# Kernel optimization log

Measured on AMD Instinct MI355X. Metric: run time of the kernel, lower is better.

Reference implementation:

```python
import jax, jax.numpy as jnp
import numpy as np

LN_EPS = 1e-5
MIN_MASK_SUM = 1e-6


def setup_inputs() -> dict:
    key = jax.random.key(0)
    ks = jax.random.split(key, 8)
    B, N, D = 8, 576, 1024
    K, H, W = 64, 512, 512
    OUT, GEOM = 256, 5
    feature_map = jax.random.normal(ks[0], (B, N, D), dtype=jnp.float32)
    masks = jax.random.randint(ks[1], (B, K, H, W), 0, 2).astype(bool)
    s = 0.02
    w1 = jax.random.normal(ks[2], (D + GEOM, OUT), dtype=jnp.float32) * s
    b1 = jnp.zeros((OUT,), dtype=jnp.float32)
    ln_g = jnp.ones((OUT,), dtype=jnp.float32)
    ln_b = jnp.zeros((OUT,), dtype=jnp.float32)
    w2 = jax.random.normal(ks[3], (OUT, OUT), dtype=jnp.float32) * s
    b2 = jnp.zeros((OUT,), dtype=jnp.float32)
    return {"feature_map": feature_map, "masks": masks, "w1": w1, "b1": b1,
            "ln_g": ln_g, "ln_b": ln_b, "w2": w2, "b2": b2}


def _geom(masks):
    # masks: [B,K,H,W] bool -> [B,K,5] (cx, cy, area_norm, bbox_w, bbox_h)
    B, K, H, W = masks.shape
    mf = masks.astype(jnp.float32)
    area = mf.sum((-2, -1))                                  # [B,K]
    xg = jnp.arange(W, dtype=jnp.float32)
    yg = jnp.arange(H, dtype=jnp.float32)
    safe = jnp.maximum(area, 1.0)
    cx = jnp.einsum('bkhw,w->bk', mf, xg) / safe / W
    cy = jnp.einsum('bkhw,h->bk', mf, yg) / safe / H
    xs_any = masks.any(axis=2)                               # [B,K,W]
    ys_any = masks.any(axis=3)                               # [B,K,H]
    xi = jnp.arange(W, dtype=jnp.int32)
    yi = jnp.arange(H, dtype=jnp.int32)
    BIG = jnp.int32(1 << 30)
    xmin = jnp.min(jnp.where(xs_any, xi, BIG), -1)
    xmax = jnp.max(jnp.where(xs_any, xi, -1), -1)
    ymin = jnp.min(jnp.where(ys_any, yi, BIG), -1)
    ymax = jnp.max(jnp.where(ys_any, yi, -1), -1)
    bw = (xmax - xmin + 1).astype(jnp.float32) / W
    bh = (ymax - ymin + 1).astype(jnp.float32) / H
    geom = jnp.stack([cx, cy, area / (H * W), bw, bh], -1)   # [B,K,5]
    return jnp.where((area >= 1.0)[..., None], geom, 0.0)


def reference(feature_map, masks, w1, b1, ln_g, ln_b, w2, b2):
    B, N, D = feature_map.shape
    _, K, H, W = masks.shape
    Hf = int(round(N ** 0.5))
    # nearest-neighbor downsample of masks to the patch grid (torch 'nearest')
    ri = (jnp.arange(Hf) * H) // Hf
    ci = (jnp.arange(Hf) * W) // Hf
    m_small = masks[:, :, ri][:, :, :, ci].astype(jnp.float32).reshape(B, K, -1)  # [B,K,N]
    msum = jnp.maximum(m_small.sum(-1, keepdims=True), MIN_MASK_SUM)
    pooled = jnp.einsum('bkn,bnd->bkd', m_small, feature_map) / msum              # [B,K,D]
    pooled = pooled - feature_map.mean(axis=1, keepdims=True)                     # bg subtract
    geom = _geom(masks)                                                           # [B,K,5]
    x = jnp.concatenate([pooled, geom], axis=-1)                                  # [B,K,D+5]
    h = jax.nn.gelu(x @ w1 + b1, approximate=False)
    mu = h.mean(-1, keepdims=True)
    var = jnp.mean((h - mu) ** 2, axis=-1, keepdims=True)
    h = (h - mu) * jax.lax.rsqrt(var + LN_EPS) * ln_g + ln_b
    return h @ w2 + b2                                                            # [B,K,out]
```

## Files before the change

kernel.cpp:

```cpp
#include <hip/hip_runtime.h>
#include <math.h>

#define BB 8
#define NN 576
#define DD 1024
#define KK 64
#define HH 512
#define WW 512
#define OUTD 256
#define HF 24
#define XSTRIDE 1032

typedef int iv4 __attribute__((ext_vector_type(4)));

__global__ __launch_bounds__(1024) void k_geom(const int* __restrict__ masks,
                                               const float* __restrict__ fm,
                                               float* __restrict__ xbuf) {
    int bid = blockIdx.x;
    int b = bid & 7;
    int k = bid >> 3;
    int bk = b * KK + k;
    int tid = threadIdx.x;
    const int* mb = masks + (size_t)bk * (HH * WW);
    const iv4* mp = (const iv4*)mb;

    __shared__ float ms[NN];
    __shared__ float s_inv;
    __shared__ float rsum[16];

    float msv = 0.f;
    if (tid < NN) {
        int i = tid / HF, j = tid - i * HF;
        int ri = (i * HH) / HF, ci = (j * WW) / HF;
        msv = (mb[ri * WW + ci] != 0) ? 1.f : 0.f;
        ms[tid] = msv;
    }
    {
        float v = msv;
        for (int off = 32; off > 0; off >>= 1) v += __shfl_down(v, off);
        if ((tid & 63) == 0) rsum[tid >> 6] = v;
    }
    __syncthreads();
    if (tid == 0) {
        float s = 0.f;
        for (int i = 0; i < 16; ++i) s += rsum[i];
        s_inv = 1.0f / fmaxf(s, 1e-6f);
    }
    __syncthreads();

    const int y0 = tid >> 7;
    const int xb = (tid & 127) << 2;
    int cnt = 0, w3a = 0, syr = 0, colany = 0;
    int ymn_it = 1 << 20, ymx_it = -1;
    float acc = 0.f, facc = 0.f;

    auto STREAM = [&]() {
        #pragma unroll 8
        for (int it = 0; it < 64; ++it) {
            iv4 m = __builtin_nontemporal_load(&mp[tid + (it << 10)]);
            int sum4 = m.x + m.y + m.z + m.w;
            int mask4 = m.x | (m.y << 1) | (m.z << 2) | (m.w << 3);
            cnt += sum4;
            w3a += m.y + (m.z << 1) + ((m.w << 1) + m.w);
            syr += sum4 * it;
            colany |= mask4;
            if (mask4) { ymn_it = min(ymn_it, it); ymx_it = it; }
        }
    };
    auto POOL = [&]() {
        const float* fp = fm + (size_t)b * NN * DD + tid;
        for (int n = 0; n < NN; n += 4) {
            float4 mq = *(const float4*)&ms[n];
            float f0 = fp[(size_t)(n + 0) * DD];
            float f1 = fp[(size_t)(n + 1) * DD];
            float f2 = fp[(size_t)(n + 2) * DD];
            float f3 = fp[(size_t)(n + 3) * DD];
            facc += f0 + f1 + f2 + f3;
            acc = fmaf(mq.x, f0, acc);
            acc = fmaf(mq.y, f1, acc);
            acc = fmaf(mq.z, f2, acc);
            acc = fmaf(mq.w, f3, acc);
        }
    };

    if (((bid ^ (bid >> 8)) & 1) == 0) { STREAM(); POOL(); }
    else                               { POOL(); STREAM(); }

    {
        float* xp = xbuf + (size_t)bk * XSTRIDE;
        xp[tid] = acc * s_inv - facc * (1.0f / 576.0f);
    }

    int sx = xb * cnt + w3a;
    int sy = (syr << 3) + y0 * cnt;
    int xmn = colany ? xb + __builtin_ctz((unsigned)colany) : (1 << 30);
    int xmx = colany ? xb + (31 - __builtin_clz((unsigned)colany)) : -1;
    int ymn = (ymx_it >= 0) ? (ymn_it << 3) + y0 : (1 << 30);
    int ymx = (ymx_it >= 0) ? (ymx_it << 3) + y0 : -1;

    for (int off = 32; off > 0; off >>= 1) {
        cnt += __shfl_down(cnt, off);
        sx  += __shfl_down(sx,  off);
        sy  += __shfl_down(sy,  off);
        xmn = min(xmn, __shfl_down(xmn, off));
        xmx = max(xmx, __shfl_down(xmx, off));
        ymn = min(ymn, __shfl_down(ymn, off));
        ymx = max(ymx, __shfl_down(ymx, off));
    }
    __shared__ int r0[16], r1[16], r2[16], r3[16], r4[16], r5[16], r6[16];
    int wv = tid >> 6;
    if ((tid & 63) == 0) {
        r0[wv] = cnt; r1[wv] = sx; r2[wv] = sy;
        r3[wv] = xmn; r4[wv] = xmx; r5[wv] = ymn; r6[wv] = ymx;
    }
    __syncthreads();
    if (tid == 0) {
        for (int i = 1; i < 16; ++i) {
            cnt += r0[i]; sx += r1[i]; sy += r2[i];
            xmn = min(xmn, r3[i]); xmx = max(xmx, r4[i]);
            ymn = min(ymn, r5[i]); ymx = max(ymx, r6[i]);
        }
        float* gp = xbuf + (size_t)bk * XSTRIDE + DD;
        if (cnt >= 1) {
            float area = (float)cnt;
            gp[0] = (float)sx / area * (1.0f / 512.0f);
            gp[1] = (float)sy / area * (1.0f / 512.0f);
            gp[2] = area * (1.0f / 262144.0f);
            gp[3] = (float)(xmx - xmn + 1) * (1.0f / 512.0f);
            gp[4] = (float)(ymx - ymn + 1) * (1.0f / 512.0f);
        } else {
            gp[0] = 0.f; gp[1] = 0.f; gp[2] = 0.f; gp[3] = 0.f; gp[4] = 0.f;
        }
        gp[5] = 0.f; gp[6] = 0.f; gp[7] = 0.f;
    }
}

__global__ __launch_bounds__(512) void k_mlp(const float* __restrict__ xbuf,
                                             const float* __restrict__ w1,
                                             const float* __restrict__ b1,
                                             const float* __restrict__ ln_g,
                                             const float* __restrict__ ln_b,
                                             const float* __restrict__ w2,
                                             const float* __restrict__ b2,
                                             float* __restrict__ out) {
    int row0 = blockIdx.x * 4;
    int tid = threadIdx.x;
    int w = tid >> 6, lane = tid & 63;
    int c4 = lane * 4;
    int col = tid & 255, rhalf = tid >> 8;

    __shared__ float xs[4][XSTRIDE];
    __shared__ float hp[8][4][OUTD];
    __shared__ float hs[4][OUTD];

    for (int i = tid; i < 4 * (XSTRIDE / 4); i += 512) {
        int r = i / (XSTRIDE / 4), cq = i % (XSTRIDE / 4);
        *(float4*)&xs[r][cq * 4] =
            *(const float4*)&xbuf[(size_t)(row0 + r) * XSTRIDE + cq * 4];
    }
    __syncthreads();

    float acc[4][4] = {};
    int js = w * 128;
    int je = (w == 7) ? 1029 : js + 128;
    int j = js;
    for (; j + 4 <= je; j += 4) {
        float4 xv0 = *(const float4*)&xs[0][j];
        float4 xv1 = *(const float4*)&xs[1][j];
        float4 xv2 = *(const float4*)&xs[2][j];
        float4 xv3 = *(const float4*)&xs[3][j];
#define STEPA(jj, X0, X1, X2, X3)                                              \
        {                                                                      \
            float4 wv = *(const float4*)&w1[(size_t)(j + jj) * OUTD + c4];     \
            acc[0][0] += X0 * wv.x; acc[0][1] += X0 * wv.y;                    \
            acc[0][2] += X0 * wv.z; acc[0][3] += X0 * wv.w;                    \
            acc[1][0] += X1 * wv.x; acc[1][1] += X1 * wv.y;                    \
            acc[1][2] += X1 * wv.z; acc[1][3] += X1 * wv.w;                    \
            acc[2][0] += X2 * wv.x; acc[2][1] += X2 * wv.y;                    \
            acc[2][2] += X2 * wv.z; acc[2][3] += X2 * wv.w;                    \
            acc[3][0] += X3 * wv.x; acc[3][1] += X3 * wv.y;                    \
            acc[3][2] += X3 * wv.z; acc[3][3] += X3 * wv.w;                    \
        }
        STEPA(0, xv0.x, xv1.x, xv2.x, xv3.x)
        STEPA(1, xv0.y, xv1.y, xv2.y, xv3.y)
        STEPA(2, xv0.z, xv1.z, xv2.z, xv3.z)
        STEPA(3, xv0.w, xv1.w, xv2.w, xv3.w)
    }
    for (; j < je; ++j) {
        float xv[4] = {xs[0][j], xs[1][j], xs[2][j], xs[3][j]};
        #pragma unroll
        for (int ci = 0; ci < 4; ++ci) {
            float wvv = w1[(size_t)j * OUTD + c4 + ci];
            #pragma unroll
            for (int r = 0; r < 4; ++r) acc[r][ci] += xv[r] * wvv;
        }
    }
    #pragma unroll
    for (int r = 0; r < 4; ++r)
        *(float4*)&hp[w][r][c4] = make_float4(acc[r][0], acc[r][1], acc[r][2], acc[r][3]);
    __syncthreads();

    float h2[2];
    float b1v = b1[col];
    #pragma unroll
    for (int r2 = 0; r2 < 2; ++r2) {
        int r = rhalf * 2 + r2;
        float s = b1v;
        #pragma unroll
        for (int ww = 0; ww < 8; ++ww) s += hp[ww][r][col];
        h2[r2] = 0.5f * s * (1.0f + erff(s * 0.70710678118654752f));
    }
    __shared__ float s1[8][2], s2[8][2];
    #pragma unroll
    for (int r2 = 0; r2 < 2; ++r2) {
        float a = h2[r2], q = h2[r2] * h2[r2];
        for (int off = 32; off > 0; off >>= 1) {
            a += __shfl_down(a, off);
            q += __shfl_down(q, off);
        }
        if (lane == 0) { s1[w][r2] = a; s2[w][r2] = q; }
    }
    __syncthreads();
    __shared__ float mu_[4], rsd_[4];
    if (tid < 4) {
        int rh = tid >> 1, r2 = tid & 1;
        float a = 0.f, q = 0.f;
        #pragma unroll
        for (int i = 0; i < 4; ++i) {
            a += s1[rh * 4 + i][r2];
            q += s2[rh * 4 + i][r2];
        }
        float mu = a * (1.0f / 256.0f);
        float var = q * (1.0f / 256.0f) - mu * mu;
        mu_[tid] = mu;
        rsd_[tid] = rsqrtf(var + 1e-5f);
    }
    __syncthreads();
    float gv = ln_g[col], bv = ln_b[col];
    #pragma unroll
    for (int r2 = 0; r2 < 2; ++r2) {
        int r = rhalf * 2 + r2;
        hs[r][col] = (h2[r2] - mu_[r]) * rsd_[r] * gv + bv;
    }
    __syncthreads();

    float a2[4][4] = {};
    int j2 = w * 32;
    for (int g = 0; g < 8; ++g, j2 += 4) {
        float4 h0 = *(const float4*)&hs[0][j2];
        float4 h1 = *(const float4*)&hs[1][j2];
        float4 h2v = *(const float4*)&hs[2][j2];
        float4 h3 = *(const float4*)&hs[3][j2];
#define STEPB(jj, X0, X1, X2, X3)                                              \
        {                                                                      \
            float4 wv = *(const float4*)&w2[(size_t)(j2 + jj) * OUTD + c4];    \
            a2[0][0] += X0 * wv.x; a2[0][1] += X0 * wv.y;                      \
            a2[0][2] += X0 * wv.z; a2[0][3] += X0 * wv.w;                      \
            a2[1][0] += X1 * wv.x; a2[1][1] += X1 * wv.y;                      \
            a2[1][2] += X1 * wv.z; a2[1][3] += X1 * wv.w;                      \
            a2[2][0] += X2 * wv.x; a2[2][1] += X2 * wv.y;                      \
            a2[2][2] += X2 * wv.z; a2[2][3] += X2 * wv.w;                      \
            a2[3][0] += X3 * wv.x; a2[3][1] += X3 * wv.y;                      \
            a2[3][2] += X3 * wv.z; a2[3][3] += X3 * wv.w;                      \
        }
        STEPB(0, h0.x, h1.x, h2v.x, h3.x)
        STEPB(1, h0.y, h1.y, h2v.y, h3.y)
        STEPB(2, h0.z, h1.z, h2v.z, h3.z)
        STEPB(3, h0.w, h1.w, h2v.w, h3.w)
    }
    #pragma unroll
    for (int r = 0; r < 4; ++r)
        *(float4*)&hp[w][r][c4] = make_float4(a2[r][0], a2[r][1], a2[r][2], a2[r][3]);
    __syncthreads();

    float b2v = b2[col];
    #pragma unroll
    for (int r2 = 0; r2 < 2; ++r2) {
        int r = rhalf * 2 + r2;
        float o = b2v;
        #pragma unroll
        for (int ww = 0; ww < 8; ++ww) o += hp[ww][r][col];
        out[(size_t)(row0 + r) * OUTD + col] = o;
    }
}

extern "C" void kernel_launch(void* const* d_in, const int* in_sizes, int n_in,
                              void* d_out, int out_size, void* d_ws, size_t ws_size,
                              hipStream_t stream) {
    const float* fm    = (const float*)d_in[0];
    const int*   masks = (const int*)d_in[1];
    const float* w1    = (const float*)d_in[2];
    const float* b1    = (const float*)d_in[3];
    const float* ln_g  = (const float*)d_in[4];
    const float* ln_b  = (const float*)d_in[5];
    const float* w2    = (const float*)d_in[6];
    const float* b2    = (const float*)d_in[7];
    float* out = (float*)d_out;

    float* xbuf = (float*)d_ws;

    k_geom<<<512, 1024, 0, stream>>>(masks, fm, xbuf);
    k_mlp <<<128, 512, 0, stream>>>(xbuf, w1, b1, ln_g, ln_b, w2, b2, out);
}
```

Before: 131.1 us.

## Interleave mask streaming with feature pooling in a single fused loop

Replaces the two sequential phases (mask stream, then feature pooling, with the order alternating per block) with one loop of 16 chunks. Each chunk first issues four nontemporal mask loads, then does nine pooling steps over the feature map, then consumes the mask registers. The aim is to hide mask-load latency behind pooling loads and arithmetic within each wave. It raises register pressure and drops the per-block phase alternation that had spread traffic between the two streams.

```diff
diff --git a/kernel.cpp b/kernel.cpp
--- a/kernel.cpp
+++ b/kernel.cpp
@@ -24,7 +24,7 @@
     const int* mb = masks + (size_t)bk * (HH * WW);
     const iv4* mp = (const iv4*)mb;
 
-    __shared__ float ms[NN];
+    __shared__ __align__(16) float ms[NN];
     __shared__ float s_inv;
     __shared__ float rsum[16];
 
@@ -54,10 +54,33 @@
     int ymn_it = 1 << 20, ymx_it = -1;
     float acc = 0.f, facc = 0.f;
 
-    auto STREAM = [&]() {
-        #pragma unroll 8
-        for (int it = 0; it < 64; ++it) {
-            iv4 m = __builtin_nontemporal_load(&mp[tid + (it << 10)]);
+    const float* fp = fm + (size_t)b * NN * DD + tid;
+
+    for (int ic = 0; ic < 16; ++ic) {
+        iv4 mreg[4];
+        #pragma unroll
+        for (int q = 0; q < 4; ++q)
+            mreg[q] = __builtin_nontemporal_load(&mp[tid + ((ic * 4 + q) << 10)]);
+
+        #pragma unroll
+        for (int q = 0; q < 9; ++q) {
+            int c = ic * 9 + q;
+            float4 mq = *(const float4*)&ms[c * 4];
+            float f0 = fp[(size_t)(c * 4 + 0) * DD];
+            float f1 = fp[(size_t)(c * 4 + 1) * DD];
+            float f2 = fp[(size_t)(c * 4 + 2) * DD];
+            float f3 = fp[(size_t)(c * 4 + 3) * DD];
+            facc += f0 + f1 + f2 + f3;
+            acc = fmaf(mq.x, f0, acc);
+            acc = fmaf(mq.y, f1, acc);
+            acc = fmaf(mq.z, f2, acc);
+            acc = fmaf(mq.w, f3, acc);
+        }
+
+        #pragma unroll
+        for (int q = 0; q < 4; ++q) {
+            iv4 m = mreg[q];
+            int it = ic * 4 + q;
             int sum4 = m.x + m.y + m.z + m.w;
             int mask4 = m.x | (m.y << 1) | (m.z << 2) | (m.w << 3);
             cnt += sum4;
@@ -66,25 +89,7 @@
             colany |= mask4;
             if (mask4) { ymn_it = min(ymn_it, it); ymx_it = it; }
         }
-    };
-    auto POOL = [&]() {
-        const float* fp = fm + (size_t)b * NN * DD + tid;
-        for (int n = 0; n < NN; n += 4) {
-            float4 mq = *(const float4*)&ms[n];
-            float f0 = fp[(size_t)(n + 0) * DD];
-            float f1 = fp[(size_t)(n + 1) * DD];
-            float f2 = fp[(size_t)(n + 2) * DD];
-            float f3 = fp[(size_t)(n + 3) * DD];
-            facc += f0 + f1 + f2 + f3;
-            acc = fmaf(mq.x, f0, acc);
-            acc = fmaf(mq.y, f1, acc);
-            acc = fmaf(mq.z, f2, acc);
-            acc = fmaf(mq.w, f3, acc);
-        }
-    };
-
-    if (((bid ^ (bid >> 8)) & 1) == 0) { STREAM(); POOL(); }
-    else                               { POOL(); STREAM(); }
+    }
 
     {
         float* xp = xbuf + (size_t)bk * XSTRIDE;
```

Result: slower. 163.2 us (+24.5%).
